# Kernel optimization log

Measured on AMD Instinct MI355X. Metric: run time of the kernel, lower is better.

Reference implementation:

```python
import jax, jax.numpy as jnp
import numpy as np

N = 100000
E = 1600000
IN_C = 128
HID = 128
N_FACTORS = 3
N_SKILLS = 7
NEG_SLOPE = 0.2


def setup_inputs() -> dict:
    key = jax.random.key(0)
    ks = jax.random.split(key, 16)
    inp = {
        "x": jax.random.normal(ks[0], (N, IN_C), dtype=jnp.float32),
        "edge_index": jax.random.randint(ks[1], (2, E), 0, N, dtype=jnp.int64),
        # GAT layer 1
        "W1": jax.random.normal(ks[2], (HID, IN_C), dtype=jnp.float32) * (1.0 / np.sqrt(IN_C)),
        "a_src1": jax.random.normal(ks[3], (HID,), dtype=jnp.float32) * 0.1,
        "a_dst1": jax.random.normal(ks[4], (HID,), dtype=jnp.float32) * 0.1,
        "b1": jnp.zeros((HID,), dtype=jnp.float32),
        # GAT layer 2
        "W2": jax.random.normal(ks[5], (HID, HID), dtype=jnp.float32) * (1.0 / np.sqrt(HID)),
        "a_src2": jax.random.normal(ks[6], (HID,), dtype=jnp.float32) * 0.1,
        "a_dst2": jax.random.normal(ks[7], (HID,), dtype=jnp.float32) * 0.1,
        "b2": jnp.zeros((HID,), dtype=jnp.float32),
        # classifier heads
        "Wf": jax.random.normal(ks[8], (N_FACTORS, HID), dtype=jnp.float32) * (1.0 / np.sqrt(HID)),
        "bf": jnp.zeros((N_FACTORS,), dtype=jnp.float32),
        "Ws": jax.random.normal(ks[9], (N_SKILLS, HID), dtype=jnp.float32) * (1.0 / np.sqrt(HID)),
        "bs": jnp.zeros((N_SKILLS,), dtype=jnp.float32),
    }
    return inp


def _gat_layer(x, src, dst, W, a_src, a_dst, b):
    # x: [N, Fin] -> h: [N, Fout]; single-head GATConv (PyG defaults)
    n = x.shape[0]
    h = x @ W.T
    alpha_s = h @ a_src  # [N]
    alpha_d = h @ a_dst  # [N]
    e = jax.nn.leaky_relu(alpha_s[src] + alpha_d[dst], NEG_SLOPE)  # [E']
    # segment softmax over incoming edges of each dst node
    emax = jax.ops.segment_max(e, dst, num_segments=n)
    w = jnp.exp(e - emax[dst])
    denom = jax.ops.segment_sum(w, dst, num_segments=n)
    alpha = w / denom[dst]
    out = jax.ops.segment_sum(h[src] * alpha[:, None], dst, num_segments=n)
    return out + b


def reference(x, edge_index, W1, a_src1, a_dst1, b1, W2, a_src2, a_dst2, b2, Wf, bf, Ws, bs):
    # add self loops (PyG GATConv default add_self_loops=True)
    loops = jnp.arange(N, dtype=edge_index.dtype)
    src = jnp.concatenate([edge_index[0], loops])
    dst = jnp.concatenate([edge_index[1], loops])

    h = jax.nn.relu(_gat_layer(x, src, dst, W1, a_src1, a_dst1, b1))
    h = jax.nn.relu(_gat_layer(h, src, dst, W2, a_src2, a_dst2, b2))
    # dropout inactive in eval mode
    factors = h @ Wf.T + bf
    skills = h @ Ws.T + bs
    return (factors, skills)
```

## Files before the change

### kernel.cpp

```cpp
#include <hip/hip_runtime.h>
#include <hip/hip_bf16.h>
#include <hip/hip_fp16.h>
#include <math.h>

#define EPB 8192
#define BPB 256

__device__ inline float sum16(float v) {
#pragma unroll
  for (int off = 1; off < 16; off <<= 1) v += __shfl_xor(v, off);
  return v;
}

typedef _Float16 h2v __attribute__((ext_vector_type(2)));
__device__ inline float fdot2u(unsigned a, unsigned b, float c) {
#if defined(__has_builtin)
#if __has_builtin(__builtin_amdgcn_fdot2)
  return __builtin_amdgcn_fdot2(*(h2v*)&a, *(h2v*)&b, c, false);
#else
  float2 fa = __half22float2(*(__half2*)&a), fb = __half22float2(*(__half2*)&b);
  return fmaf(fa.x, fb.x, fmaf(fa.y, fb.y, c));
#endif
#else
  float2 fa = __half22float2(*(__half2*)&a), fb = __half22float2(*(__half2*)&b);
  return fmaf(fa.x, fb.x, fmaf(fa.y, fb.y, c));
#endif
}

__device__ inline uint2 load4h(const float* p) {
  float4 v = *(const float4*)p;
  union { __half2 h[2]; uint2 u; } pk;
  pk.h[0] = __floats2half2_rn(v.x, v.y);
  pk.h[1] = __floats2half2_rn(v.z, v.w);
  return pk.u;
}
__device__ inline uint2 load4h(const __half* p) { return *(const uint2*)p; }

__global__ void k_scan1(const int* __restrict__ in, int* out, int* bsum, int n) {
  __shared__ int s[256];
  int t = threadIdx.x;
  int base = blockIdx.x * 1024 + t * 4;
  int v[4];
  int sum = 0;
#pragma unroll
  for (int i = 0; i < 4; ++i) {
    v[i] = (base + i < n) ? in[base + i] : 0;
    sum += v[i];
  }
  s[t] = sum;
  __syncthreads();
  for (int off = 1; off < 256; off <<= 1) {
    int x = (t >= off) ? s[t - off] : 0;
    __syncthreads();
    s[t] += x;
    __syncthreads();
  }
  int excl = s[t] - sum;
  if (t == 255) bsum[blockIdx.x] = s[255];
  int run = excl;
#pragma unroll
  for (int i = 0; i < 4; ++i) {
    if (base + i < n) out[base + i] = run;
    run += v[i];
  }
}

__global__ void k_scan2(int* bsum, int nb) {
  __shared__ int s[256];
  int t = threadIdx.x;
  int v = (t < nb) ? bsum[t] : 0;
  s[t] = v;
  __syncthreads();
  for (int off = 1; off < 256; off <<= 1) {
    int x = (t >= off) ? s[t - off] : 0;
    __syncthreads();
    s[t] += x;
    __syncthreads();
  }
  if (t == nb - 1) bsum[256] = s[t];
  __syncthreads();
  if (t < nb) bsum[t] = s[t] - v;
}

__global__ void k_scan3(int* out, const int* __restrict__ bsum, int n) {
  int i = blockIdx.x * 256 + threadIdx.x;
  if (i < n) out[i] += bsum[i >> 10];
  if (i == 0) out[n] = bsum[256];
}

__global__ __launch_bounds__(256) void k_pcount(const int* __restrict__ ei, int* cnt,
                                                int nE, int n, int PB, int NB) {
  __shared__ int hist[512];
  int p = blockIdx.x, t = threadIdx.x;
  for (int i = t; i < NB; i += 256) hist[i] = 0;
  __syncthreads();
  int e0 = p * EPB;
  int e1 = min(e0 + EPB, nE);
  for (int i = e0 + t; i < e1; i += 256) {
    int d = ei[nE + i];
    if ((unsigned)d < (unsigned)n) atomicAdd(&hist[d >> 8], 1);
  }
  __syncthreads();
  for (int i = t; i < NB; i += 256) cnt[i * PB + p] = hist[i];
}

__global__ __launch_bounds__(256) void k_ppart(const int* __restrict__ ei,
                                               const int* __restrict__ cscan,
                                               int2* __restrict__ part,
                                               int nE, int n, int PB, int NB) {
  __shared__ int cur[512];
  int p = blockIdx.x, t = threadIdx.x;
  for (int i = t; i < NB; i += 256) cur[i] = cscan[i * PB + p];
  __syncthreads();
  int e0 = p * EPB;
  int e1 = min(e0 + EPB, nE);
  for (int i = e0 + t; i < e1; i += 256) {
    int d = ei[nE + i];
    int s = ei[i];
    if ((unsigned)d < (unsigned)n) {
      int pos = atomicAdd(&cur[d >> 8], 1);
      part[pos] = make_int2(s, d);
    }
  }
}

__global__ __launch_bounds__(256) void k_bucket(const int2* __restrict__ part,
                                                const int* __restrict__ cscan,
                                                int* __restrict__ rowptr,
                                                int* __restrict__ col,
                                                int PB, int NB, int n) {
  __shared__ int sdeg[256];
  __shared__ int sscan[256];
  __shared__ int lcol[8448];
  int b = blockIdx.x, t = threadIdx.x;
  int node0 = b * BPB;
  int ebeg = cscan[b * PB];
  int eend = (b == NB - 1) ? cscan[NB * PB] : cscan[(b + 1) * PB];
  int cnt = eend - ebeg;
  if (cnt > 8192) cnt = 8192;
  int nloc = n - node0;
  if (nloc > BPB) nloc = BPB;

  sdeg[t] = (t < nloc) ? 1 : 0;
  __syncthreads();
  for (int i = t; i < cnt; i += 256) {
    int d = part[ebeg + i].y;
    atomicAdd(&sdeg[d - node0], 1);
  }
  __syncthreads();
  int v = sdeg[t];
  sscan[t] = v;
  __syncthreads();
  for (int off = 1; off < 256; off <<= 1) {
    int x = (t >= off) ? sscan[t - off] : 0;
    __syncthreads();
    sscan[t] += x;
    __syncthreads();
  }
  int excl = sscan[t] - v;
  int gbase = ebeg + node0;
  if (t < nloc) rowptr[node0 + t] = gbase + excl;
  if (b == NB - 1 && t == 0) rowptr[n] = cscan[NB * PB] + n;
  if (t < nloc) lcol[excl] = node0 + t;
  sdeg[t] = excl + 1;
  __syncthreads();
  for (int i = t; i < cnt; i += 256) {
    int2 e = part[ebeg + i];
    int pos = atomicAdd(&sdeg[e.y - node0], 1);
    lcol[pos] = e.x;
  }
  __syncthreads();
  int T = cnt + nloc;
  for (int i = t; i < T; i += 256) col[gbase + i] = lcol[i];
}

template <typename T>
__global__ __launch_bounds__(256) void k_linear128(const T* __restrict__ X,
                                                   const float* __restrict__ W,
                                                   const float* __restrict__ a_src,
                                                   const float* __restrict__ a_dst,
                                                   __half* __restrict__ H16,
                                                   float* __restrict__ as_,
                                                   float* __restrict__ ad_, int nrows) {
  __shared__ uint2 Xs2[64 * 32];
  __shared__ uint2 Ws2[64 * 32];
  int t = threadIdx.x;
  int row0 = blockIdx.x * 64;
  int rg = t >> 4;
  int cg = t & 15;
  int rgl = rg & 3;

#pragma unroll
  for (int i = 0; i < 8; ++i) {
    int idx = t + i * 256;
    int r = idx >> 5;
    int kc = idx & 31;
    uint2 u = make_uint2(0u, 0u);
    if (row0 + r < nrows) u = load4h(&X[(size_t)(row0 + r) * 128 + kc * 4]);
    Xs2[r * 32 + (kc ^ ((r >> 2) & 3))] = u;
  }

  float asum[4] = {0.f, 0.f, 0.f, 0.f};
  float adsum[4] = {0.f, 0.f, 0.f, 0.f};

#pragma unroll
  for (int half = 0; half < 2; ++half) {
    if (half == 1) __syncthreads();
    const float* Wh = W + (size_t)half * 64 * 128;
#pragma unroll
    for (int i = 0; i < 8; ++i) {
      int idx = t + i * 256;
      int c = idx >> 5;
      int kc = idx & 31;
      Ws2[c * 32 + (kc ^ ((c >> 2) & 15))] = load4h(&Wh[(size_t)c * 128 + kc * 4]);
    }
    __syncthreads();

    float acc[4][4];
#pragma unroll
    for (int i = 0; i < 4; ++i)
#pragma unroll
      for (int j = 0; j < 4; ++j) acc[i][j] = 0.f;

#pragma unroll 8
    for (int k4 = 0; k4 < 32; ++k4) {
      int sx = k4 ^ rgl;
      int sw = k4 ^ cg;
      uint2 xv[4], wv[4];
#pragma unroll
      for (int i = 0; i < 4; ++i) xv[i] = Xs2[(rg * 4 + i) * 32 + sx];
#pragma unroll
      for (int j = 0; j < 4; ++j) wv[j] = Ws2[(cg * 4 + j) * 32 + sw];
#pragma unroll
      for (int i = 0; i < 4; ++i)
#pragma unroll
        for (int j = 0; j < 4; ++j) {
          acc[i][j] = fdot2u(xv[i].x, wv[j].x, acc[i][j]);
          acc[i][j] = fdot2u(xv[i].y, wv[j].y, acc[i][j]);
        }
    }

    int c0 = half * 64 + cg * 4;
    float4 av = *(const float4*)&a_src[c0];
    float4 dv = *(const float4*)&a_dst[c0];
#pragma unroll
    for (int i = 0; i < 4; ++i) {
      int r = row0 + rg * 4 + i;
      if (r < nrows) {
        union { __half2 h2[2]; uint2 u; } pk;
        pk.h2[0] = __floats2half2_rn(acc[i][0], acc[i][1]);
        pk.h2[1] = __floats2half2_rn(acc[i][2], acc[i][3]);
        *(uint2*)&H16[(size_t)r * 128 + c0] = pk.u;
      }
      asum[i] += acc[i][0] * av.x + acc[i][1] * av.y + acc[i][2] * av.z + acc[i][3] * av.w;
      adsum[i] += acc[i][0] * dv.x + acc[i][1] * dv.y + acc[i][2] * dv.z + acc[i][3] * dv.w;
    }
  }

#pragma unroll
  for (int i = 0; i < 4; ++i) {
    asum[i] = sum16(asum[i]);
    adsum[i] = sum16(adsum[i]);
  }
  if (cg == 0) {
#pragma unroll
    for (int i = 0; i < 4; ++i) {
      int r = row0 + rg * 4 + i;
      if (r < nrows) {
        as_[r] = asum[i];
        ad_[r] = adsum[i];
      }
    }
  }
}

#define AGG_SLOT(K, QREG)                                                  \
  if (K == 0 || jj + K < trips) {                                          \
    float wj = __shfl(wgt, gb | (jj + K));                                 \
    uint4 cur = QREG;                                                      \
    if (jj + K + 4 < trips) {                                              \
      int sq = __shfl(s, gb | (jj + K + 4));                               \
      QREG = *(const uint4*)(h + (size_t)sq * 128 + li * 8);               \
    }                                                                      \
    float2 f0 = __half22float2(*(__half2*)&cur.x);                         \
    float2 f1 = __half22float2(*(__half2*)&cur.y);                         \
    float2 f2 = __half22float2(*(__half2*)&cur.z);                         \
    float2 f3 = __half22float2(*(__half2*)&cur.w);                         \
    acc0 = fmaf(f0.x, wj, acc0); acc1 = fmaf(f0.y, wj, acc1);              \
    acc2 = fmaf(f1.x, wj, acc2); acc3 = fmaf(f1.y, wj, acc3);              \
    acc4 = fmaf(f2.x, wj, acc4); acc5 = fmaf(f2.y, wj, acc5);              \
    acc6 = fmaf(f3.x, wj, acc6); acc7 = fmaf(f3.y, wj, acc7);              \
  }

template <bool HEADS>
__global__ __launch_bounds__(256) void k_agg_t(const __half* __restrict__ h,
                                               const float* __restrict__ as_,
                                               const float* __restrict__ ad_,
                                               const int* __restrict__ rowptr,
                                               const int* __restrict__ col,
                                               const float* __restrict__ bias,
                                               void* __restrict__ outp,
                                               const float* __restrict__ Wf,
                                               const float* __restrict__ bf,
                                               const float* __restrict__ Wsk,
                                               const float* __restrict__ bs,
                                               int n) {
  int gid = blockIdx.x * 256 + threadIdx.x;
  int wid = gid >> 6;
  int lane = gid & 63;
  int g = lane >> 4;
  int li = lane & 15;
  int gb = lane & 48;
  int node = wid * 4 + g;
  bool valid = node < n;
  int beg = 0, end = 0;
  float adv = 0.f;
  if (valid) {
    beg = rowptr[node];
    end = rowptr[node + 1];
    adv = ad_[node];
  }
  int deg = end - beg;
  int md = deg;
  md = max(md, __shfl_xor(md, 16));
  md = max(md, __shfl_xor(md, 32));

  float acc0 = 0.f, acc1 = 0.f, acc2 = 0.f, acc3 = 0.f;
  float acc4 = 0.f, acc5 = 0.f, acc6 = 0.f, acc7 = 0.f;
  float den_l = 0.f;

  for (int base = 0; base < md; base += 16) {
    int s = 0;
    float wgt = 0.f;
    if (base + li < deg) {
      s = col[beg + base + li];
      if ((unsigned)s >= (unsigned)n) s = 0;
      float v = as_[s] + adv;
      v = (v > 0.f) ? v : 0.2f * v;
      wgt = __expf(v);
    }
    den_l += wgt;

    int rem = md - base;
    int trips = rem > 16 ? 16 : rem;
    uint4 q0 = make_uint4(0u, 0u, 0u, 0u);
    uint4 q1 = q0, q2 = q0, q3 = q0;
    {
      int sq = __shfl(s, gb);
      q0 = *(const uint4*)(h + (size_t)sq * 128 + li * 8);
      if (trips > 1) { sq = __shfl(s, gb | 1); q1 = *(const uint4*)(h + (size_t)sq * 128 + li * 8); }
      if (trips > 2) { sq = __shfl(s, gb | 2); q2 = *(const uint4*)(h + (size_t)sq * 128 + li * 8); }
      if (trips > 3) { sq = __shfl(s, gb | 3); q3 = *(const uint4*)(h + (size_t)sq * 128 + li * 8); }
    }
    for (int jj = 0; jj < trips; jj += 4) {
      AGG_SLOT(0, q0)
      AGG_SLOT(1, q1)
      AGG_SLOT(2, q2)
      AGG_SLOT(3, q3)
    }
  }

  float den = sum16(den_l);
  float inv = 1.0f / den;

  float4 bv0 = *(const float4*)&bias[li * 8];
  float4 bv1 = *(const float4*)&bias[li * 8 + 4];
  float o0 = fmaxf(fmaf(acc0, inv, bv0.x), 0.f);
  float o1 = fmaxf(fmaf(acc1, inv, bv0.y), 0.f);
  float o2 = fmaxf(fmaf(acc2, inv, bv0.z), 0.f);
  float o3 = fmaxf(fmaf(acc3, inv, bv0.w), 0.f);
  float o4 = fmaxf(fmaf(acc4, inv, bv1.x), 0.f);
  float o5 = fmaxf(fmaf(acc5, inv, bv1.y), 0.f);
  float o6 = fmaxf(fmaf(acc6, inv, bv1.z), 0.f);
  float o7 = fmaxf(fmaf(acc7, inv, bv1.w), 0.f);

  if (!HEADS) {
    if (valid) {
      union { __half2 h2[4]; uint4 u; } pk;
      pk.h2[0] = __floats2half2_rn(o0, o1);
      pk.h2[1] = __floats2half2_rn(o2, o3);
      pk.h2[2] = __floats2half2_rn(o4, o5);
      pk.h2[3] = __floats2half2_rn(o6, o7);
      *(uint4*)&(((__half*)outp)[(size_t)node * 128 + li * 8]) = pk.u;
    }
  } else {
    float p[10];
#pragma unroll
    for (int j = 0; j < 3; ++j) {
      float4 w0 = *(const float4*)&Wf[(size_t)j * 128 + li * 8];
      float4 w1 = *(const float4*)&Wf[(size_t)j * 128 + li * 8 + 4];
      p[j] = o0 * w0.x + o1 * w0.y + o2 * w0.z + o3 * w0.w +
             o4 * w1.x + o5 * w1.y + o6 * w1.z + o7 * w1.w;
    }
#pragma unroll
    for (int j = 0; j < 7; ++j) {
      float4 w0 = *(const float4*)&Wsk[(size_t)j * 128 + li * 8];
      float4 w1 = *(const float4*)&Wsk[(size_t)j * 128 + li * 8 + 4];
      p[3 + j] = o0 * w0.x + o1 * w0.y + o2 * w0.z + o3 * w0.w +
                 o4 * w1.x + o5 * w1.y + o6 * w1.z + o7 * w1.w;
    }
#pragma unroll
    for (int j = 0; j < 10; ++j) p[j] = sum16(p[j]);
    if (li == 0 && valid) {
      float* out = (float*)outp;
#pragma unroll
      for (int j = 0; j < 3; ++j) out[(size_t)node * 3 + j] = p[j] + bf[j];
      float* sk = out + (size_t)n * 3;
#pragma unroll
      for (int j = 0; j < 7; ++j) sk[(size_t)node * 7 + j] = p[3 + j] + bs[j];
    }
  }
}

extern "C" void kernel_launch(void* const* d_in, const int* in_sizes, int n_in,
                              void* d_out, int out_size, void* d_ws, size_t ws_size,
                              hipStream_t stream) {
  const float* x = (const float*)d_in[0];
  const int* ei = (const int*)d_in[1];
  const float* W1 = (const float*)d_in[2];
  const float* a_src1 = (const float*)d_in[3];
  const float* a_dst1 = (const float*)d_in[4];
  const float* b1 = (const float*)d_in[5];
  const float* W2 = (const float*)d_in[6];
  const float* a_src2 = (const float*)d_in[7];
  const float* a_dst2 = (const float*)d_in[8];
  const float* b2 = (const float*)d_in[9];
  const float* Wf = (const float*)d_in[10];
  const float* bf = (const float*)d_in[11];
  const float* Wsk = (const float*)d_in[12];
  const float* bs = (const float*)d_in[13];
  float* out = (float*)d_out;

  const int N = in_sizes[0] / 128;
  const int nE = in_sizes[1] / 2;
  const int NB = (N + BPB - 1) / BPB;
  const int PB = (nE + EPB - 1) / EPB;
  const int NCNT = NB * PB;

  char* w = (char*)d_ws;
  auto carve = [&](size_t bytes) {
    char* p = w;
    w += (bytes + 255) & ~(size_t)255;
    return (void*)p;
  };
  __half* H16 = (__half*)carve((size_t)N * 128 * 2);
  __half* B16 = (__half*)carve((size_t)N * 128 * 2);
  float* as_ = (float*)carve((size_t)N * 4);
  float* ad_ = (float*)carve((size_t)N * 4);
  int* rowptr = (int*)carve((size_t)(N + 1) * 4);
  int* col = (int*)carve((size_t)(nE + N) * 4);
  int* cnt_raw = (int*)carve((size_t)NCNT * 4);
  int* cnt_scan = (int*)carve((size_t)(NCNT + 1) * 4);
  int* bsum = (int*)carve(512 * 4);
  int2* part = (int2*)carve((size_t)nE * 8);

  dim3 b256(256);
  const int nb_scan = (NCNT + 1023) / 1024;

  k_pcount<<<PB, b256, 0, stream>>>(ei, cnt_raw, nE, N, PB, NB);
  k_scan1<<<nb_scan, b256, 0, stream>>>(cnt_raw, cnt_scan, bsum, NCNT);
  k_scan2<<<1, b256, 0, stream>>>(bsum, nb_scan);
  k_scan3<<<(NCNT + 255) / 256, b256, 0, stream>>>(cnt_scan, bsum, NCNT);
  k_ppart<<<PB, b256, 0, stream>>>(ei, cnt_scan, part, nE, N, PB, NB);
  k_bucket<<<NB, b256, 0, stream>>>(part, cnt_scan, rowptr, col, PB, NB, N);

  const int gemm_blocks = (N + 63) / 64;
  const int agg_blocks = (((N + 3) / 4) * 64 + 255) / 256;

  k_linear128<float><<<gemm_blocks, b256, 0, stream>>>(x, W1, a_src1, a_dst1, H16, as_, ad_, N);
  k_agg_t<false><<<agg_blocks, b256, 0, stream>>>(H16, as_, ad_, rowptr, col, b1, B16,
                                                  nullptr, nullptr, nullptr, nullptr, N);

  k_linear128<__half><<<gemm_blocks, b256, 0, stream>>>(B16, W2, a_src2, a_dst2, H16, as_, ad_, N);
  k_agg_t<true><<<agg_blocks, b256, 0, stream>>>(H16, as_, ad_, rowptr, col, b2, out,
                                                 Wf, bf, Wsk, bs, N);
}
```

Measured before the change: 390.3 us.

## Use MFMA for node linear transform and simplify CSR bucket offset scan

Replaces the fdot2-based SIMT GEMM with a kernel using MFMA 16x16x32 f16 instructions, loading all of W into shared memory once instead of in two halves. The attention logits are computed from the MFMA accumulators. Separately, the multi-kernel scan over per-block counts is replaced by global atomics that assign per-block offsets, followed by a single small scan over bucket totals, which cuts several launches. The atomic offset order is nondeterministic, so edge order within a bucket can vary between runs.

```diff
diff --git a/kernel.cpp b/kernel.cpp
--- a/kernel.cpp
+++ b/kernel.cpp
@@ -6,47 +6,56 @@
 #define EPB 8192
 #define BPB 256
 
+typedef _Float16 v8h __attribute__((ext_vector_type(8)));
+typedef float v4f __attribute__((ext_vector_type(4)));
+
 __device__ inline float sum16(float v) {
 #pragma unroll
   for (int off = 1; off < 16; off <<= 1) v += __shfl_xor(v, off);
   return v;
 }
 
-typedef _Float16 h2v __attribute__((ext_vector_type(2)));
-__device__ inline float fdot2u(unsigned a, unsigned b, float c) {
-#if defined(__has_builtin)
-#if __has_builtin(__builtin_amdgcn_fdot2)
-  return __builtin_amdgcn_fdot2(*(h2v*)&a, *(h2v*)&b, c, false);
-#else
-  float2 fa = __half22float2(*(__half2*)&a), fb = __half22float2(*(__half2*)&b);
-  return fmaf(fa.x, fb.x, fmaf(fa.y, fb.y, c));
-#endif
-#else
-  float2 fa = __half22float2(*(__half2*)&a), fb = __half22float2(*(__half2*)&b);
-  return fmaf(fa.x, fb.x, fmaf(fa.y, fb.y, c));
-#endif
-}
-
-__device__ inline uint2 load4h(const float* p) {
-  float4 v = *(const float4*)p;
-  union { __half2 h[2]; uint2 u; } pk;
-  pk.h[0] = __floats2half2_rn(v.x, v.y);
-  pk.h[1] = __floats2half2_rn(v.z, v.w);
+__device__ inline uint4 load8h(const float* p) {
+  float4 a = *(const float4*)p;
+  float4 b = *(const float4*)(p + 4);
+  union { __half2 h[4]; uint4 u; } pk;
+  pk.h[0] = __floats2half2_rn(a.x, a.y);
+  pk.h[1] = __floats2half2_rn(a.z, a.w);
+  pk.h[2] = __floats2half2_rn(b.x, b.y);
+  pk.h[3] = __floats2half2_rn(b.z, b.w);
   return pk.u;
 }
-__device__ inline uint2 load4h(const __half* p) { return *(const uint2*)p; }
-
-__global__ void k_scan1(const int* __restrict__ in, int* out, int* bsum, int n) {
+__device__ inline uint4 load8h(const __half* p) { return *(const uint4*)p; }
+
+__global__ __launch_bounds__(256) void k_pcount(const int* __restrict__ ei,
+                                                int* __restrict__ btot,
+                                                int* __restrict__ blkoff,
+                                                int nE, int n, int PB, int NB) {
+  __shared__ int hist[512];
+  int p = blockIdx.x, t = threadIdx.x;
+  for (int i = t; i < NB; i += 256) hist[i] = 0;
+  __syncthreads();
+  int e0 = p * EPB;
+  int e1 = min(e0 + EPB, nE);
+  for (int i = e0 + t; i < e1; i += 256) {
+    int d = ei[nE + i];
+    if ((unsigned)d < (unsigned)n) atomicAdd(&hist[d >> 8], 1);
+  }
+  __syncthreads();
+  for (int i = t; i < NB; i += 256) {
+    int h = hist[i];
+    int off = atomicAdd(&btot[i], h);
+    blkoff[i * PB + p] = off;
+  }
+}
+
+__global__ __launch_bounds__(256) void k_bscan(const int* __restrict__ btot,
+                                               int* __restrict__ bbase, int NB) {
   __shared__ int s[256];
   int t = threadIdx.x;
-  int base = blockIdx.x * 1024 + t * 4;
-  int v[4];
-  int sum = 0;
-#pragma unroll
-  for (int i = 0; i < 4; ++i) {
-    v[i] = (base + i < n) ? in[base + i] : 0;
-    sum += v[i];
-  }
+  int v0 = (2 * t < NB) ? btot[2 * t] : 0;
+  int v1 = (2 * t + 1 < NB) ? btot[2 * t + 1] : 0;
+  int sum = v0 + v1;
   s[t] = sum;
   __syncthreads();
   for (int off = 1; off < 256; off <<= 1) {
@@ -56,61 +65,19 @@
     __syncthreads();
   }
   int excl = s[t] - sum;
-  if (t == 255) bsum[blockIdx.x] = s[255];
-  int run = excl;
-#pragma unroll
-  for (int i = 0; i < 4; ++i) {
-    if (base + i < n) out[base + i] = run;
-    run += v[i];
-  }
-}
-
-__global__ void k_scan2(int* bsum, int nb) {
-  __shared__ int s[256];
-  int t = threadIdx.x;
-  int v = (t < nb) ? bsum[t] : 0;
-  s[t] = v;
-  __syncthreads();
-  for (int off = 1; off < 256; off <<= 1) {
-    int x = (t >= off) ? s[t - off] : 0;
-    __syncthreads();
-    s[t] += x;
-    __syncthreads();
-  }
-  if (t == nb - 1) bsum[256] = s[t];
-  __syncthreads();
-  if (t < nb) bsum[t] = s[t] - v;
-}
-
-__global__ void k_scan3(int* out, const int* __restrict__ bsum, int n) {
-  int i = blockIdx.x * 256 + threadIdx.x;
-  if (i < n) out[i] += bsum[i >> 10];
-  if (i == 0) out[n] = bsum[256];
-}
-
-__global__ __launch_bounds__(256) void k_pcount(const int* __restrict__ ei, int* cnt,
-                                                int nE, int n, int PB, int NB) {
-  __shared__ int hist[512];
-  int p = blockIdx.x, t = threadIdx.x;
-  for (int i = t; i < NB; i += 256) hist[i] = 0;
-  __syncthreads();
-  int e0 = p * EPB;
-  int e1 = min(e0 + EPB, nE);
-  for (int i = e0 + t; i < e1; i += 256) {
-    int d = ei[nE + i];
-    if ((unsigned)d < (unsigned)n) atomicAdd(&hist[d >> 8], 1);
-  }
-  __syncthreads();
-  for (int i = t; i < NB; i += 256) cnt[i * PB + p] = hist[i];
+  if (2 * t < NB) bbase[2 * t] = excl;
+  if (2 * t + 1 < NB) bbase[2 * t + 1] = excl + v0;
+  if (t == 0) bbase[NB] = s[255];
 }
 
 __global__ __launch_bounds__(256) void k_ppart(const int* __restrict__ ei,
-                                               const int* __restrict__ cscan,
+                                               const int* __restrict__ bbase,
+                                               const int* __restrict__ blkoff,
                                                int2* __restrict__ part,
                                                int nE, int n, int PB, int NB) {
   __shared__ int cur[512];
   int p = blockIdx.x, t = threadIdx.x;
-  for (int i = t; i < NB; i += 256) cur[i] = cscan[i * PB + p];
+  for (int i = t; i < NB; i += 256) cur[i] = bbase[i] + blkoff[i * PB + p];
   __syncthreads();
   int e0 = p * EPB;
   int e1 = min(e0 + EPB, nE);
@@ -125,17 +92,17 @@
 }
 
 __global__ __launch_bounds__(256) void k_bucket(const int2* __restrict__ part,
-                                                const int* __restrict__ cscan,
+                                                const int* __restrict__ bbase,
                                                 int* __restrict__ rowptr,
                                                 int* __restrict__ col,
-                                                int PB, int NB, int n) {
+                                                int NB, int n) {
   __shared__ int sdeg[256];
   __shared__ int sscan[256];
   __shared__ int lcol[8448];
   int b = blockIdx.x, t = threadIdx.x;
   int node0 = b * BPB;
-  int ebeg = cscan[b * PB];
-  int eend = (b == NB - 1) ? cscan[NB * PB] : cscan[(b + 1) * PB];
+  int ebeg = bbase[b];
+  int eend = bbase[b + 1];
   int cnt = eend - ebeg;
   if (cnt > 8192) cnt = 8192;
   int nloc = n - node0;
@@ -160,7 +127,7 @@
   int excl = sscan[t] - v;
   int gbase = ebeg + node0;
   if (t < nloc) rowptr[node0 + t] = gbase + excl;
-  if (b == NB - 1 && t == 0) rowptr[n] = cscan[NB * PB] + n;
+  if (b == NB - 1 && t == 0) rowptr[n] = bbase[NB] + n;
   if (t < nloc) lcol[excl] = node0 + t;
   sdeg[t] = excl + 1;
   __syncthreads();
@@ -175,100 +142,98 @@
 }
 
 template <typename T>
-__global__ __launch_bounds__(256) void k_linear128(const T* __restrict__ X,
-                                                   const float* __restrict__ W,
-                                                   const float* __restrict__ a_src,
-                                                   const float* __restrict__ a_dst,
-                                                   __half* __restrict__ H16,
-                                                   float* __restrict__ as_,
-                                                   float* __restrict__ ad_, int nrows) {
-  __shared__ uint2 Xs2[64 * 32];
-  __shared__ uint2 Ws2[64 * 32];
+__global__ __launch_bounds__(256) void k_linear_mfma(const T* __restrict__ X,
+                                                     const float* __restrict__ W,
+                                                     const float* __restrict__ a_src,
+                                                     const float* __restrict__ a_dst,
+                                                     __half* __restrict__ H16,
+                                                     float* __restrict__ as_,
+                                                     float* __restrict__ ad_, int nrows) {
+  __shared__ uint4 Xs[64 * 16];
+  __shared__ uint4 Ws[128 * 16];
   int t = threadIdx.x;
   int row0 = blockIdx.x * 64;
-  int rg = t >> 4;
-  int cg = t & 15;
-  int rgl = rg & 3;
-
+
+#pragma unroll
+  for (int i = 0; i < 4; ++i) {
+    int idx = t + i * 256;
+    int r = idx >> 4;
+    int j = idx & 15;
+    uint4 u = make_uint4(0u, 0u, 0u, 0u);
+    if (row0 + r < nrows) u = load8h(&X[(size_t)(row0 + r) * 128 + j * 8]);
+    Xs[r * 16 + (j ^ (r & 15))] = u;
+  }
 #pragma unroll
   for (int i = 0; i < 8; ++i) {
     int idx = t + i * 256;
-    int r = idx >> 5;
-    int kc = idx & 31;
-    uint2 u = make_uint2(0u, 0u);
-    if (row0 + r < nrows) u = load4h(&X[(size_t)(row0 + r) * 128 + kc * 4]);
-    Xs2[r * 32 + (kc ^ ((r >> 2) & 3))] = u;
+    int c = idx >> 4;
+    int j = idx & 15;
+    Ws[c * 16 + (j ^ (c & 15))] = load8h(&W[(size_t)c * 128 + j * 8]);
+  }
+  __syncthreads();
+
+  int w = t >> 6;
+  int lane = t & 63;
+  int li = lane & 15;
+  int quad = lane >> 4;
+
+  v4f acc[8];
+#pragma unroll
+  for (int ct = 0; ct < 8; ++ct) acc[ct] = (v4f){0.f, 0.f, 0.f, 0.f};
+
+#pragma unroll
+  for (int kk = 0; kk < 4; ++kk) {
+    int ch = (kk * 4 + quad);
+    union { uint4 u; v8h h; } av;
+    av.u = Xs[(w * 16 + li) * 16 + (ch ^ li)];
+#pragma unroll
+    for (int ct = 0; ct < 8; ++ct) {
+      union { uint4 u; v8h h; } bv;
+      bv.u = Ws[(ct * 16 + li) * 16 + (ch ^ li)];
+      acc[ct] = __builtin_amdgcn_mfma_f32_16x16x32_f16(av.h, bv.h, acc[ct], 0, 0, 0);
+    }
   }
 
   float asum[4] = {0.f, 0.f, 0.f, 0.f};
   float adsum[4] = {0.f, 0.f, 0.f, 0.f};
-
-#pragma unroll
-  for (int half = 0; half < 2; ++half) {
-    if (half == 1) __syncthreads();
-    const float* Wh = W + (size_t)half * 64 * 128;
-#pragma unroll
-    for (int i = 0; i < 8; ++i) {
-      int idx = t + i * 256;
-      int c = idx >> 5;
-      int kc = idx & 31;
-      Ws2[c * 32 + (kc ^ ((c >> 2) & 15))] = load4h(&Wh[(size_t)c * 128 + kc * 4]);
-    }
-    __syncthreads();
-
-    float acc[4][4];
-#pragma unroll
-    for (int i = 0; i < 4; ++i)
-#pragma unroll
-      for (int j = 0; j < 4; ++j) acc[i][j] = 0.f;
-
-#pragma unroll 8
-    for (int k4 = 0; k4 < 32; ++k4) {
-      int sx = k4 ^ rgl;
-      int sw = k4 ^ cg;
-      uint2 xv[4], wv[4];
-#pragma unroll
-      for (int i = 0; i < 4; ++i) xv[i] = Xs2[(rg * 4 + i) * 32 + sx];
-#pragma unroll
-      for (int j = 0; j < 4; ++j) wv[j] = Ws2[(cg * 4 + j) * 32 + sw];
-#pragma unroll
-      for (int i = 0; i < 4; ++i)
-#pragma unroll
-        for (int j = 0; j < 4; ++j) {
-          acc[i][j] = fdot2u(xv[i].x, wv[j].x, acc[i][j]);
-          acc[i][j] = fdot2u(xv[i].y, wv[j].y, acc[i][j]);
+#pragma unroll
+  for (int ct = 0; ct < 8; ++ct) {
+    float sa = a_src[ct * 16 + li];
+    float da = a_dst[ct * 16 + li];
+#pragma unroll
+    for (int reg = 0; reg < 4; ++reg) {
+      asum[reg] = fmaf(acc[ct][reg], sa, asum[reg]);
+      adsum[reg] = fmaf(acc[ct][reg], da, adsum[reg]);
+    }
+  }
+#pragma unroll
+  for (int reg = 0; reg < 4; ++reg) {
+    asum[reg] = sum16(asum[reg]);
+    adsum[reg] = sum16(adsum[reg]);
+  }
+  if (li == 0) {
+#pragma unroll
+    for (int reg = 0; reg < 4; ++reg) {
+      int r = row0 + w * 16 + quad * 4 + reg;
+      if (r < nrows) {
+        as_[r] = asum[reg];
+        ad_[r] = adsum[reg];
+      }
+    }
+  }
+
+#pragma unroll
+  for (int ct = 0; ct < 8; ++ct) {
+#pragma unroll
+    for (int reg = 0; reg < 4; ++reg) {
+      float v0 = acc[ct][reg];
+      float v1 = __shfl_xor(v0, 1);
+      if (!(li & 1)) {
+        int r = row0 + w * 16 + quad * 4 + reg;
+        if (r < nrows) {
+          __half2 hh = __floats2half2_rn(v0, v1);
+          *(__half2*)&H16[(size_t)r * 128 + ct * 16 + li] = hh;
         }
-    }
-
-    int c0 = half * 64 + cg * 4;
-    float4 av = *(const float4*)&a_src[c0];
-    float4 dv = *(const float4*)&a_dst[c0];
-#pragma unroll
-    for (int i = 0; i < 4; ++i) {
-      int r = row0 + rg * 4 + i;
-      if (r < nrows) {
-        union { __half2 h2[2]; uint2 u; } pk;
-        pk.h2[0] = __floats2half2_rn(acc[i][0], acc[i][1]);
-        pk.h2[1] = __floats2half2_rn(acc[i][2], acc[i][3]);
-        *(uint2*)&H16[(size_t)r * 128 + c0] = pk.u;
-      }
-      asum[i] += acc[i][0] * av.x + acc[i][1] * av.y + acc[i][2] * av.z + acc[i][3] * av.w;
-      adsum[i] += acc[i][0] * dv.x + acc[i][1] * dv.y + acc[i][2] * dv.z + acc[i][3] * dv.w;
-    }
-  }
-
-#pragma unroll
-  for (int i = 0; i < 4; ++i) {
-    asum[i] = sum16(asum[i]);
-    adsum[i] = sum16(adsum[i]);
-  }
-  if (cg == 0) {
-#pragma unroll
-    for (int i = 0; i < 4; ++i) {
-      int r = row0 + rg * 4 + i;
-      if (r < nrows) {
-        as_[r] = asum[i];
-        ad_[r] = adsum[i];
       }
     }
   }
@@ -449,29 +414,27 @@
   float* ad_ = (float*)carve((size_t)N * 4);
   int* rowptr = (int*)carve((size_t)(N + 1) * 4);
   int* col = (int*)carve((size_t)(nE + N) * 4);
-  int* cnt_raw = (int*)carve((size_t)NCNT * 4);
-  int* cnt_scan = (int*)carve((size_t)(NCNT + 1) * 4);
-  int* bsum = (int*)carve(512 * 4);
+  int* btot = (int*)carve((size_t)(NB + 1) * 4);
+  int* bbase = (int*)carve((size_t)(NB + 1) * 4);
+  int* blkoff = (int*)carve((size_t)NCNT * 4);
   int2* part = (int2*)carve((size_t)nE * 8);
 
   dim3 b256(256);
-  const int nb_scan = (NCNT + 1023) / 1024;
-
-  k_pcount<<<PB, b256, 0, stream>>>(ei, cnt_raw, nE, N, PB, NB);
-  k_scan1<<<nb_scan, b256, 0, stream>>>(cnt_raw, cnt_scan, bsum, NCNT);
-  k_scan2<<<1, b256, 0, stream>>>(bsum, nb_scan);
-  k_scan3<<<(NCNT + 255) / 256, b256, 0, stream>>>(cnt_scan, bsum, NCNT);
-  k_ppart<<<PB, b256, 0, stream>>>(ei, cnt_scan, part, nE, N, PB, NB);
-  k_bucket<<<NB, b256, 0, stream>>>(part, cnt_scan, rowptr, col, PB, NB, N);
+
+  hipMemsetAsync(btot, 0, (size_t)(NB + 1) * 4, stream);
+  k_pcount<<<PB, b256, 0, stream>>>(ei, btot, blkoff, nE, N, PB, NB);
+  k_bscan<<<1, b256, 0, stream>>>(btot, bbase, NB);
+  k_ppart<<<PB, b256, 0, stream>>>(ei, bbase, blkoff, part, nE, N, PB, NB);
+  k_bucket<<<NB, b256, 0, stream>>>(part, bbase, rowptr, col, NB, N);
 
   const int gemm_blocks = (N + 63) / 64;
   const int agg_blocks = (((N + 3) / 4) * 64 + 255) / 256;
 
-  k_linear128<float><<<gemm_blocks, b256, 0, stream>>>(x, W1, a_src1, a_dst1, H16, as_, ad_, N);
+  k_linear_mfma<float><<<gemm_blocks, b256, 0, stream>>>(x, W1, a_src1, a_dst1, H16, as_, ad_, N);
   k_agg_t<false><<<agg_blocks, b256, 0, stream>>>(H16, as_, ad_, rowptr, col, b1, B16,
                                                   nullptr, nullptr, nullptr, nullptr, N);
 
-  k_linear128<__half><<<gemm_blocks, b256, 0, stream>>>(B16, W2, a_src2, a_dst2, H16, as_, ad_, N);
+  k_linear_mfma<__half><<<gemm_blocks, b256, 0, stream>>>(B16, W2, a_src2, a_dst2, H16, as_, ad_, N);
   k_agg_t<true><<<agg_blocks, b256, 0, stream>>>(H16, as_, ad_, rowptr, col, b2, out,
                                                  Wf, bf, Wsk, bs, N);
 }
```

Result: faster. 342.8 us (-12.2%).
